# Optimization experiments

Measured on AMD Instinct MI355X. Metric: run time of the kernel, lower is better.

The kernel has to match this reference:

```python
import jax, jax.numpy as jnp
import numpy as np

N_NODES = 500_000
N_EDGES = 16_000_000


def setup_inputs() -> dict:
    key = jax.random.key(0)
    ks = jax.random.split(key, 16)
    x = jax.random.normal(ks[0], (N_NODES, 4), dtype=jnp.float32)
    edge_index = jax.random.randint(ks[1], (2, N_EDGES), 0, N_NODES, dtype=jnp.int64)

    def lin(k, out_dim, in_dim):
        # kaiming-uniform-ish init like torch Linear
        bound = 1.0 / np.sqrt(in_dim)
        return jax.random.uniform(k, (out_dim, in_dim), jnp.float32, -bound, bound)

    def bias(k, out_dim, in_dim):
        bound = 1.0 / np.sqrt(in_dim)
        return jax.random.uniform(k, (out_dim,), jnp.float32, -bound, bound)

    return {
        "x": x,
        "edge_index": edge_index,
        # SAGEConv1: 4 -> 10  (lin_l acts on aggregated neighbors, has bias; lin_r on self, no bias)
        "w1l": lin(ks[2], 10, 4), "b1": bias(ks[3], 10, 4), "w1r": lin(ks[4], 10, 4),
        # SAGEConv2: 10 -> 20
        "w2l": lin(ks[5], 20, 10), "b2": bias(ks[6], 20, 10), "w2r": lin(ks[7], 20, 10),
        # SAGEConv3: 20 -> 20
        "w3l": lin(ks[8], 20, 20), "b3": bias(ks[9], 20, 20), "w3r": lin(ks[10], 20, 20),
        # classifier: 20 -> 8
        "wc": lin(ks[11], 8, 20), "bc": bias(ks[12], 8, 20),
    }


def _sage_conv(h, src, dst, deg_inv, wl, bl, wr):
    # mean-aggregate neighbor features: messages flow src -> dst
    msg = h[src]                                   # [E, F] gather
    agg = jax.ops.segment_sum(msg, dst, num_segments=N_NODES)  # [N, F]
    agg = agg * deg_inv                            # mean over in-neighbors
    return agg @ wl.T + bl + h @ wr.T              # lin_l(aggr) + lin_r(self)


def reference(x, edge_index, w1l, b1, w1r, w2l, b2, w2r, w3l, b3, w3r, wc, bc):
    src, dst = edge_index[0], edge_index[1]
    deg = jax.ops.segment_sum(jnp.ones((src.shape[0],), x.dtype), dst,
                              num_segments=N_NODES)
    deg_inv = (1.0 / jnp.maximum(deg, 1.0))[:, None]  # [N, 1]

    h = jax.nn.relu(_sage_conv(x, src, dst, deg_inv, w1l, b1, w1r))
    h = jax.nn.relu(_sage_conv(h, src, dst, deg_inv, w2l, b2, w2r))
    h = jax.nn.relu(_sage_conv(h, src, dst, deg_inv, w3l, b3, w3r))
    return h @ wc.T + bc
```

## Files before the change

### kernel.cpp

```cpp
#include <hip/hip_runtime.h>
#include <hip/hip_fp16.h>

#define N_NODES 500000
#define N_EDGES 16000000
#define NB 1954
#define NPB_LOG 9
#define NPB 512
#define NBUCK 977
#define NBUCK_PAD 1024
#define CH 32768
#define NSB 489

#define SLICE_SHIFT 15
#define NSLICE 16
#define NKEY (NPB * NSLICE)

__device__ __forceinline__ float2 up2(int p) {
    __half2 h = *reinterpret_cast<__half2*>(&p);
    return __half22float2(h);
}
__device__ __forceinline__ int pk2(float a, float b) {
    __half2 h = __floats2half2_rn(a, b);
    return *reinterpret_cast<int*>(&h);
}


__global__ void bucket_hist(const int* __restrict__ dst, int* __restrict__ ghist) {
    __shared__ int lhist[NBUCK_PAD];
    for (int t = threadIdx.x; t < NBUCK_PAD; t += 256) lhist[t] = 0;
    __syncthreads();
    int stride = gridDim.x * 256;
    for (int i = blockIdx.x * 256 + threadIdx.x; i < N_EDGES; i += stride) {
        atomicAdd(&lhist[dst[i] >> NPB_LOG], 1);
    }
    __syncthreads();
    for (int t = threadIdx.x; t < NBUCK_PAD; t += 256) {
        int c = lhist[t];
        if (c) atomicAdd(&ghist[t], c);
    }
}

__global__ void bucket_scan(int* __restrict__ gcur, int* __restrict__ bbase) {
    __shared__ int s[256];
    int t = threadIdx.x;
    int v[4], sum = 0, loc[4];
#pragma unroll
    for (int j = 0; j < 4; ++j) {
        v[j] = gcur[t * 4 + j];
        loc[j] = sum;
        sum += v[j];
    }
    s[t] = sum;
    __syncthreads();
    for (int o = 1; o < 256; o <<= 1) {
        int x = (t >= o) ? s[t - o] : 0;
        __syncthreads();
// ... 77 lines not shown
    }
    __syncthreads();

#pragma unroll
    for (int j = 0; j < 2; ++j) {
        int idx = t + j * 256;
        int ng = node0 + idx;
        if (ng < N_NODES) off[ng] = bb + hist[idx << 4];
    }
    if (b == NBUCK - 1 && t == 0) off[N_NODES] = N_EDGES;
    __syncthreads();

    for (int j = bb + t; j < be; j += 256) {
        int p = P[j];
        int n = p >> 19;
        int s = p & 0x7FFFF;
        int pos = atomicAdd(&hist[(n << 4) | (s >> SLICE_SHIFT)], 1);
        S[bb + pos] = s;
    }
}


__global__ void convert_x(const float* __restrict__ x, int2* __restrict__ xh) {
    int i = blockIdx.x * 256 + threadIdx.x;
    if (i >= N_NODES) return;
    float4 v = ((const float4*)x)[i];
    int2 r;
    r.x = pk2(v.x, v.y);
    r.y = pk2(v.z, v.w);
    xh[i] = r;
}


__global__ __launch_bounds__(256, 4) void fused_l1(
        const int* __restrict__ off, const int* __restrict__ ssrc,
        const int2* __restrict__ xh, const float* __restrict__ x,
        const float* __restrict__ wl, const float* __restrict__ bl,
        const float* __restrict__ wr, int* __restrict__ h1) {
    __shared__ float s_wl[40];
    __shared__ float s_wr[40];
    __shared__ float s_b[10];
    if (threadIdx.x < 40) {
        s_wl[threadIdx.x] = wl[threadIdx.x];
        s_wr[threadIdx.x] = wr[threadIdx.x];
    }
    if (threadIdx.x >= 64 && threadIdx.x < 74) s_b[threadIdx.x - 64] = bl[threadIdx.x - 64];
    __syncthreads();

    int i = blockIdx.x * 256 + threadIdx.x;
    if (i >= N_NODES) return;

    int b = off[i], e = off[i + 1];
    constexpr int UN = 8;

    float acc[4] = {0.f, 0.f, 0.f, 0.f};

    int k = b;
    for (; k + UN - 1 < e; k += UN) {
        int sidx[UN];
#pragma unroll
        for (int u = 0; u < UN; ++u) sidx[u] = ssrc[k + u];
        int2 v[UN];
#pragma unroll
        for (int u = 0; u < UN; ++u) v[u] = xh[sidx[u]];
#pragma unroll
        for (int u = 0; u < UN; ++u) {
            float2 f0 = up2(v[u].x), f1 = up2(v[u].y);
            acc[0] += f0.x; acc[1] += f0.y; acc[2] += f1.x; acc[3] += f1.y;
        }
    }
    for (; k < e; ++k) {
        int2 v = xh[ssrc[k]];
        float2 f0 = up2(v.x), f1 = up2(v.y);
        acc[0] += f0.x; acc[1] += f0.y; acc[2] += f1.x; acc[3] += f1.y;
    }

    float inv = 1.f / fmaxf((float)(e - b), 1.f);
#pragma unroll
    for (int q = 0; q < 4; ++q) acc[q] *= inv;

    float4 xs = ((const float4*)x)[i];
    float xv[4] = {xs.x, xs.y, xs.z, xs.w};

    float r[10];
#pragma unroll
    for (int j = 0; j < 10; ++j) {
        float t = s_b[j];
#pragma unroll
        for (int kk = 0; kk < 4; ++kk) {
            t += s_wl[j * 4 + kk] * acc[kk] + s_wr[j * 4 + kk] * xv[kk];
        }
        r[j] = fmaxf(t, 0.f);
    }
    int4 o0;
    o0.x = pk2(r[0], r[1]); o0.y = pk2(r[2], r[3]);
    o0.z = pk2(r[4], r[5]); o0.w = pk2(r[6], r[7]);
    *(int4*)(h1 + (long)i * 8) = o0;
    h1[(long)i * 8 + 4] = pk2(r[8], r[9]);
}

__global__ __launch_bounds__(256, 4) void fused_l2(
        const int* __restrict__ off, const int* __restrict__ ssrc,
        const int* __restrict__ h1,
        const float* __restrict__ wl, const float* __restrict__ bl,
        const float* __restrict__ wr, int* __restrict__ h2) {
    __shared__ float s_wl[200];
    __shared__ float s_wr[200];
    __shared__ float s_b[20];
    if (threadIdx.x < 200) {
        s_wl[threadIdx.x] = wl[threadIdx.x];
        s_wr[threadIdx.x] = wr[threadIdx.x];
    }
    if (threadIdx.x >= 224 && threadIdx.x < 244) s_b[threadIdx.x - 224] = bl[threadIdx.x - 224];
    __syncthreads();

    int i = blockIdx.x * 256 + threadIdx.x;
    if (i >= N_NODES) return;

    int b = off[i], e = off[i + 1];
    constexpr int UN = 4;

    float acc[10];
#pragma unroll
    for (int q = 0; q < 10; ++q) acc[q] = 0.f;

    int k = b;
    for (; k + UN - 1 < e; k += UN) {
        int sidx[UN];
#pragma unroll
        for (int u = 0; u < UN; ++u) sidx[u] = ssrc[k + u];
        int4 v4[UN];
        int v1[UN];
#pragma unroll
        for (int u = 0; u < UN; ++u) {
            const int* row = h1 + (long)sidx[u] * 8;
            v4[u] = *(const int4*)row;
            v1[u] = row[4];
        }
#pragma unroll
        for (int u = 0; u < UN; ++u) {
            float2 f0 = up2(v4[u].x), f1 = up2(v4[u].y), f2 = up2(v4[u].z), f3 = up2(v4[u].w), f4 = up2(v1[u]);
            acc[0] += f0.x; acc[1] += f0.y; acc[2] += f1.x; acc[3] += f1.y;
            acc[4] += f2.x; acc[5] += f2.y; acc[6] += f3.x; acc[7] += f3.y;
            acc[8] += f4.x; acc[9] += f4.y;
        }
    }
    for (; k < e; ++k) {
        const int* row = h1 + (long)ssrc[k] * 8;
        int4 v4 = *(const int4*)row;
        int v1 = row[4];
        float2 f0 = up2(v4.x), f1 = up2(v4.y), f2 = up2(v4.z), f3 = up2(v4.w), f4 = up2(v1);
        acc[0] += f0.x; acc[1] += f0.y; acc[2] += f1.x; acc[3] += f1.y;
        acc[4] += f2.x; acc[5] += f2.y; acc[6] += f3.x; acc[7] += f3.y;
        acc[8] += f4.x; acc[9] += f4.y;
    }

    float inv = 1.f / fmaxf((float)(e - b), 1.f);
#pragma unroll
    for (int q = 0; q < 10; ++q) acc[q] *= inv;

    float xv[10];
    {
        const int* row = h1 + (long)i * 8;
        int4 v4 = *(const int4*)row;
        int v1 = row[4];
        float2 f0 = up2(v4.x), f1 = up2(v4.y), f2 = up2(v4.z), f3 = up2(v4.w), f4 = up2(v1);
        xv[0] = f0.x; xv[1] = f0.y; xv[2] = f1.x; xv[3] = f1.y;
        xv[4] = f2.x; xv[5] = f2.y; xv[6] = f3.x; xv[7] = f3.y;
        xv[8] = f4.x; xv[9] = f4.y;
    }

    float r[20];
#pragma unroll
    for (int j = 0; j < 20; ++j) {
        float t = s_b[j];
#pragma unroll
        for (int kk = 0; kk < 10; ++kk) {
            t += s_wl[j * 10 + kk] * acc[kk] + s_wr[j * 10 + kk] * xv[kk];
        }
        r[j] = fmaxf(t, 0.f);
    }
    int* o = h2 + (long)i * 16;
    int4 o0, o1;
    o0.x = pk2(r[0], r[1]);   o0.y = pk2(r[2], r[3]);
    o0.z = pk2(r[4], r[5]);   o0.w = pk2(r[6], r[7]);
    o1.x = pk2(r[8], r[9]);   o1.y = pk2(r[10], r[11]);
    o1.z = pk2(r[12], r[13]); o1.w = pk2(r[14], r[15]);
    *(int4*)o = o0;
    *(int4*)(o + 4) = o1;
    int2 o2;
    o2.x = pk2(r[16], r[17]); o2.y = pk2(r[18], r[19]);
    *(int2*)(o + 8) = o2;
}

__global__ __launch_bounds__(256, 4) void fused_l3(
        const int* __restrict__ off, const int* __restrict__ ssrc,
        const int* __restrict__ h2,
        const float* __restrict__ w3l, const float* __restrict__ b3,
        const float* __restrict__ w3r,
        const float* __restrict__ wc, const float* __restrict__ bc,
        float* __restrict__ out) {
    __shared__ float s_wl[400];
    __shared__ float s_wr[400];
    __shared__ float s_b[20];
    __shared__ float s_wc[160];
    __shared__ float s_bc[8];
    for (int t = threadIdx.x; t < 400; t += 256) {
        s_wl[t] = w3l[t];
        s_wr[t] = w3r[t];
    }
    if (threadIdx.x < 160) s_wc[threadIdx.x] = wc[threadIdx.x];
    if (threadIdx.x >= 192 && threadIdx.x < 212) s_b[threadIdx.x - 192] = b3[threadIdx.x - 192];
    if (threadIdx.x >= 224 && threadIdx.x < 232) s_bc[threadIdx.x - 224] = bc[threadIdx.x - 224];
    __syncthreads();

    int i = blockIdx.x * 256 + threadIdx.x;
    if (i >= N_NODES) return;

    int b = off[i], e = off[i + 1];
    constexpr int UN = 4;

    float acc[20];
#pragma unroll
    for (int q = 0; q < 20; ++q) acc[q] = 0.f;

    int k = b;
    for (; k + UN - 1 < e; k += UN) {
        int sidx[UN];
#pragma unroll
        for (int u = 0; u < UN; ++u) sidx[u] = ssrc[k + u];
        int4 va[UN], vb[UN];
        int2 vc[UN];
#pragma unroll
        for (int u = 0; u < UN; ++u) {
            const int* row = h2 + (long)sidx[u] * 16;
            va[u] = *(const int4*)row;
            vb[u] = *(const int4*)(row + 4);
            vc[u] = *(const int2*)(row + 8);
        }
#pragma unroll
        for (int u = 0; u < UN; ++u) {
            float2 f;
            f = up2(va[u].x); acc[0] += f.x; acc[1] += f.y;
            f = up2(va[u].y); acc[2] += f.x; acc[3] += f.y;
            f = up2(va[u].z); acc[4] += f.x; acc[5] += f.y;
            f = up2(va[u].w); acc[6] += f.x; acc[7] += f.y;
            f = up2(vb[u].x); acc[8] += f.x; acc[9] += f.y;
            f = up2(vb[u].y); acc[10] += f.x; acc[11] += f.y;
            f = up2(vb[u].z); acc[12] += f.x; acc[13] += f.y;
            f = up2(vb[u].w); acc[14] += f.x; acc[15] += f.y;
            f = up2(vc[u].x); acc[16] += f.x; acc[17] += f.y;
            f = up2(vc[u].y); acc[18] += f.x; acc[19] += f.y;
        }
    }
    for (; k < e; ++k) {
        const int* row = h2 + (long)ssrc[k] * 16;
        int4 va = *(const int4*)row;
        int4 vb = *(const int4*)(row + 4);
        int2 vc = *(const int2*)(row + 8);
        float2 f;
        f = up2(va.x); acc[0] += f.x; acc[1] += f.y;
        f = up2(va.y); acc[2] += f.x; acc[3] += f.y;
        f = up2(va.z); acc[4] += f.x; acc[5] += f.y;
        f = up2(va.w); acc[6] += f.x; acc[7] += f.y;
        f = up2(vb.x); acc[8] += f.x; acc[9] += f.y;
        f = up2(vb.y); acc[10] += f.x; acc[11] += f.y;
        f = up2(vb.z); acc[12] += f.x; acc[13] += f.y;
        f = up2(vb.w); acc[14] += f.x; acc[15] += f.y;
        f = up2(vc.x); acc[16] += f.x; acc[17] += f.y;
        f = up2(vc.y); acc[18] += f.x; acc[19] += f.y;
    }

    float inv = 1.f / fmaxf((float)(e - b), 1.f);
#pragma unroll
    for (int q = 0; q < 20; ++q) acc[q] *= inv;

    float xv[20];
    {
        const int* row = h2 + (long)i * 16;
        int4 va = *(const int4*)row;
        int4 vb = *(const int4*)(row + 4);
        int2 vc = *(const int2*)(row + 8);
        float2 f;
        f = up2(va.x); xv[0] = f.x; xv[1] = f.y;
        f = up2(va.y); xv[2] = f.x; xv[3] = f.y;
        f = up2(va.z); xv[4] = f.x; xv[5] = f.y;
        f = up2(va.w); xv[6] = f.x; xv[7] = f.y;
        f = up2(vb.x); xv[8] = f.x; xv[9] = f.y;
        f = up2(vb.y); xv[10] = f.x; xv[11] = f.y;
        f = up2(vb.z); xv[12] = f.x; xv[13] = f.y;
        f = up2(vb.w); xv[14] = f.x; xv[15] = f.y;
        f = up2(vc.x); xv[16] = f.x; xv[17] = f.y;
        f = up2(vc.y); xv[18] = f.x; xv[19] = f.y;
    }

    float h3[20];
#pragma unroll
    for (int j = 0; j < 20; ++j) {
        float r = s_b[j];
#pragma unroll
        for (int kk = 0; kk < 20; ++kk) {
            r += s_wl[j * 20 + kk] * acc[kk] + s_wr[j * 20 + kk] * xv[kk];
        }
        h3[j] = fmaxf(r, 0.f);
    }
#pragma unroll
    for (int j = 0; j < 8; ++j) {
        float r = s_bc[j];
#pragma unroll
        for (int kk = 0; kk < 20; ++kk) {
            r += s_wc[j * 20 + kk] * h3[kk];
        }
        out[(long)i * 8 + j] = r;
    }
}


__global__ void deg_kernel(const int* __restrict__ dst, int* __restrict__ deg) {
    int i = blockIdx.x * blockDim.x + threadIdx.x;
    if (i < N_EDGES) atomicAdd(&deg[dst[i]], 1);
}

template <int F>
__global__ void edge_agg(const int* __restrict__ src, const int* __restrict__ dst,
                         const float* __restrict__ h, float* __restrict__ agg) {
    int i = blockIdx.x * blockDim.x + threadIdx.x;
    if (i >= N_EDGES) return;
    int s = src[i];
    int d = dst[i];
    const float* hs = h + (long)s * F;
    float* ad = agg + (long)d * F;
#pragma unroll
    for (int f = 0; f < F; ++f) atomicAdd(&ad[f], hs[f]);
}

template <int FIN, int FOUT>
__global__ void node_apply(const float* __restrict__ agg, const float* __restrict__ hin,
                           const int* __restrict__ deg, const float* __restrict__ wl,
                           const float* __restrict__ bl, const float* __restrict__ wr,
                           float* __restrict__ hout) {
    __shared__ float s_wl[FOUT * FIN];
    __shared__ float s_wr[FOUT * FIN];
    __shared__ float s_b[FOUT];
    for (int t = threadIdx.x; t < FOUT * FIN; t += blockDim.x) {
        s_wl[t] = wl[t];
        s_wr[t] = wr[t];
    }
// ... 69 lines not shown
    const int* ei = (const int*)d_in[1];
    const float* w1l = (const float*)d_in[2];
    const float* b1 = (const float*)d_in[3];
    const float* w1r = (const float*)d_in[4];
    const float* w2l = (const float*)d_in[5];
    const float* b2 = (const float*)d_in[6];
    const float* w2r = (const float*)d_in[7];
    const float* w3l = (const float*)d_in[8];
    const float* b3 = (const float*)d_in[9];
    const float* w3r = (const float*)d_in[10];
    const float* wc = (const float*)d_in[11];
    const float* bc = (const float*)d_in[12];
    float* out = (float*)d_out;

    const int* src = ei;
    const int* dst = ei + N_EDGES;

    const int BT = 256;
    dim3 blk(BT);
    dim3 egrid((N_EDGES + BT - 1) / BT);
    dim3 ngrid(NB);

    const size_t NEED_A = 130008448;

    if (ws_size >= NEED_A) {
        char* ws = (char*)d_ws;
        int* off = (int*)ws;
        int* bbase = (int*)(ws + 2000128);
        int* gcur = (int*)(ws + 2004352);
        int* P = (int*)(ws + 2008448);
        int2* xh = (int2*)(ws + 2008448);
        int* h1 = (int*)(ws + 6008448);
        int* h2 = (int*)(ws + 22008448);
        int* S = (int*)(ws + 66008448);

        hipMemsetAsync(gcur, 0, NBUCK_PAD * sizeof(int), stream);
        bucket_hist<<<1024, blk, 0, stream>>>(dst, gcur);
        bucket_scan<<<1, blk, 0, stream>>>(gcur, bbase);
        bucket_scatter<<<NSB, blk, 0, stream>>>(src, dst, gcur, P);
        fine_sort<<<NBUCK, blk, 0, stream>>>(P, bbase, off, S);

        convert_x<<<ngrid, blk, 0, stream>>>(x, xh);
        fused_l1<<<ngrid, blk, 0, stream>>>(off, S, xh, x, w1l, b1, w1r, h1);
        fused_l2<<<ngrid, blk, 0, stream>>>(off, S, h1, w2l, b2, w2r, h2);
        fused_l3<<<ngrid, blk, 0, stream>>>(off, S, h2, w3l, b3, w3r, wc, bc, out);
    } else {
        char* ws = (char*)d_ws;
        int* deg = (int*)ws;
        float* agg = (float*)(ws + 2000000);
        float* h1 = (float*)(ws + 42000000);
        float* h2 = (float*)(ws + 62000000);

        hipMemsetAsync(deg, 0, (size_t)N_NODES * sizeof(int), stream);
        deg_kernel<<<egrid, blk, 0, stream>>>(dst, deg);

        hipMemsetAsync(agg, 0, (size_t)N_NODES * 4 * sizeof(float), stream);
        edge_agg<4><<<egrid, blk, 0, stream>>>(src, dst, x, agg);
        node_apply<4, 10><<<ngrid, blk, 0, stream>>>(agg, x, deg, w1l, b1, w1r, h1);

        hipMemsetAsync(agg, 0, (size_t)N_NODES * 10 * sizeof(float), stream);
        edge_agg<10><<<egrid, blk, 0, stream>>>(src, dst, h1, agg);
        node_apply<10, 20><<<ngrid, blk, 0, stream>>>(agg, h1, deg, w2l, b2, w2r, h2);

        hipMemsetAsync(agg, 0, (size_t)N_NODES * 20 * sizeof(float), stream);
        edge_agg<20><<<egrid, blk, 0, stream>>>(src, dst, h2, agg);
        node_final_old<<<ngrid, blk, 0, stream>>>(agg, h2, deg, w3l, b3, w3r, wc, bc, out);
    }
}
```

Measured before the change: 1.650 ms.

## Sweep source-node slices in lockstep across grid with soft barriers for cache locality

Replaces the three per-node gather kernels with persistent-style kernels of 1024 blocks, each thread handling two destination nodes. Threads walk their sorted neighbor lists one source slice at a time, and a relaxed soft grid barrier between slices keeps all blocks on the same slice of the feature table so the gathers stay cache-resident. The barrier gives up after a spin budget, so correctness does not depend on co-residency. The cost is spin-wait overhead and lower per-thread memory parallelism, since the unrolled batched loads become serial dependent loads.

```diff
diff --git a/kernel.cpp b/kernel.cpp
--- a/kernel.cpp
+++ b/kernel.cpp
@@ -15,6 +15,9 @@
 #define NSLICE 16
 #define NKEY (NPB * NSLICE)
 
+#define GRID_BLK 1024
+#define NTHREADS (GRID_BLK * 256)
+
 __device__ __forceinline__ float2 up2(int p) {
     __half2 h = *reinterpret_cast<__half2*>(&p);
     return __half22float2(h);
@@ -22,6 +25,17 @@
 __device__ __forceinline__ int pk2(float a, float b) {
     __half2 h = __floats2half2_rn(a, b);
     return *reinterpret_cast<int*>(&h);
+}
+
+__device__ __forceinline__ bool grid_phase_barrier(int* bar, int idx, int budget, bool wait) {
+    __hip_atomic_fetch_add(&bar[idx], 1, __ATOMIC_RELAXED, __HIP_MEMORY_SCOPE_AGENT);
+    if (!wait) return false;
+    int spins = 0;
+    while (__hip_atomic_load(&bar[idx], __ATOMIC_RELAXED, __HIP_MEMORY_SCOPE_AGENT) < GRID_BLK) {
+        if (++spins > budget) return false;
+        __builtin_amdgcn_s_sleep(16);
+    }
+    return true;
 }
 
 
@@ -165,11 +179,38 @@
 }
 
 
-__global__ __launch_bounds__(256, 4) void fused_l1(
+__device__ __forceinline__ void l1_tail(int n, float deg, const float* acc,
+        const float* __restrict__ x, const float* s_wl, const float* s_wr,
+        const float* s_b, int* __restrict__ h1) {
+    if (n >= N_NODES) return;
+    float inv = 1.f / fmaxf(deg, 1.f);
+    float a[4];
+#pragma unroll
+    for (int q = 0; q < 4; ++q) a[q] = acc[q] * inv;
+    float4 xs = ((const float4*)x)[n];
+    float xv[4] = {xs.x, xs.y, xs.z, xs.w};
+    float r[10];
+#pragma unroll
+    for (int j = 0; j < 10; ++j) {
+        float t = s_b[j];
+#pragma unroll
+        for (int kk = 0; kk < 4; ++kk)
+            t += s_wl[j * 4 + kk] * a[kk] + s_wr[j * 4 + kk] * xv[kk];
+        r[j] = fmaxf(t, 0.f);
+    }
+    int4 o0;
+    o0.x = pk2(r[0], r[1]); o0.y = pk2(r[2], r[3]);
+    o0.z = pk2(r[4], r[5]); o0.w = pk2(r[6], r[7]);
+    *(int4*)(h1 + (long)n * 8) = o0;
+    h1[(long)n * 8 + 4] = pk2(r[8], r[9]);
+}
+
+__global__ __launch_bounds__(256, 4) void fused_l1p(
         const int* __restrict__ off, const int* __restrict__ ssrc,
         const int2* __restrict__ xh, const float* __restrict__ x,
         const float* __restrict__ wl, const float* __restrict__ bl,
-        const float* __restrict__ wr, int* __restrict__ h1) {
+        const float* __restrict__ wr, int* __restrict__ h1,
+        int* __restrict__ bar) {
     __shared__ float s_wl[40];
     __shared__ float s_wr[40];
     __shared__ float s_b[10];
@@ -180,121 +221,55 @@
     if (threadIdx.x >= 64 && threadIdx.x < 74) s_b[threadIdx.x - 64] = bl[threadIdx.x - 64];
     __syncthreads();
 
-    int i = blockIdx.x * 256 + threadIdx.x;
-    if (i >= N_NODES) return;
-
-    int b = off[i], e = off[i + 1];
-    constexpr int UN = 8;
-
-    float acc[4] = {0.f, 0.f, 0.f, 0.f};
-
-    int k = b;
-    for (; k + UN - 1 < e; k += UN) {
-        int sidx[UN];
-#pragma unroll
-        for (int u = 0; u < UN; ++u) sidx[u] = ssrc[k + u];
-        int2 v[UN];
-#pragma unroll
-        for (int u = 0; u < UN; ++u) v[u] = xh[sidx[u]];
-#pragma unroll
-        for (int u = 0; u < UN; ++u) {
-            float2 f0 = up2(v[u].x), f1 = up2(v[u].y);
-            acc[0] += f0.x; acc[1] += f0.y; acc[2] += f1.x; acc[3] += f1.y;
-        }
-    }
-    for (; k < e; ++k) {
-        int2 v = xh[ssrc[k]];
-        float2 f0 = up2(v.x), f1 = up2(v.y);
-        acc[0] += f0.x; acc[1] += f0.y; acc[2] += f1.x; acc[3] += f1.y;
-    }
-
-    float inv = 1.f / fmaxf((float)(e - b), 1.f);
-#pragma unroll
-    for (int q = 0; q < 4; ++q) acc[q] *= inv;
-
-    float4 xs = ((const float4*)x)[i];
-    float xv[4] = {xs.x, xs.y, xs.z, xs.w};
-
-    float r[10];
-#pragma unroll
-    for (int j = 0; j < 10; ++j) {
-        float t = s_b[j];
-#pragma unroll
-        for (int kk = 0; kk < 4; ++kk) {
-            t += s_wl[j * 4 + kk] * acc[kk] + s_wr[j * 4 + kk] * xv[kk];
-        }
-        r[j] = fmaxf(t, 0.f);
-    }
-    int4 o0;
-    o0.x = pk2(r[0], r[1]); o0.y = pk2(r[2], r[3]);
-    o0.z = pk2(r[4], r[5]); o0.w = pk2(r[6], r[7]);
-    *(int4*)(h1 + (long)i * 8) = o0;
-    h1[(long)i * 8 + 4] = pk2(r[8], r[9]);
-}
-
-__global__ __launch_bounds__(256, 4) void fused_l2(
-        const int* __restrict__ off, const int* __restrict__ ssrc,
-        const int* __restrict__ h1,
-        const float* __restrict__ wl, const float* __restrict__ bl,
-        const float* __restrict__ wr, int* __restrict__ h2) {
-    __shared__ float s_wl[200];
-    __shared__ float s_wr[200];
-    __shared__ float s_b[20];
-    if (threadIdx.x < 200) {
-        s_wl[threadIdx.x] = wl[threadIdx.x];
-        s_wr[threadIdx.x] = wr[threadIdx.x];
-    }
-    if (threadIdx.x >= 224 && threadIdx.x < 244) s_b[threadIdx.x - 224] = bl[threadIdx.x - 224];
-    __syncthreads();
-
-    int i = blockIdx.x * 256 + threadIdx.x;
-    if (i >= N_NODES) return;
-
-    int b = off[i], e = off[i + 1];
-    constexpr int UN = 4;
-
-    float acc[10];
-#pragma unroll
-    for (int q = 0; q < 10; ++q) acc[q] = 0.f;
-
-    int k = b;
-    for (; k + UN - 1 < e; k += UN) {
-        int sidx[UN];
-#pragma unroll
-        for (int u = 0; u < UN; ++u) sidx[u] = ssrc[k + u];
-        int4 v4[UN];
-        int v1[UN];
-#pragma unroll
-        for (int u = 0; u < UN; ++u) {
-            const int* row = h1 + (long)sidx[u] * 8;
-            v4[u] = *(const int4*)row;
-            v1[u] = row[4];
-        }
-#pragma unroll
-        for (int u = 0; u < UN; ++u) {
-            float2 f0 = up2(v4[u].x), f1 = up2(v4[u].y), f2 = up2(v4[u].z), f3 = up2(v4[u].w), f4 = up2(v1[u]);
-            acc[0] += f0.x; acc[1] += f0.y; acc[2] += f1.x; acc[3] += f1.y;
-            acc[4] += f2.x; acc[5] += f2.y; acc[6] += f3.x; acc[7] += f3.y;
-            acc[8] += f4.x; acc[9] += f4.y;
-        }
-    }
-    for (; k < e; ++k) {
-        const int* row = h1 + (long)ssrc[k] * 8;
-        int4 v4 = *(const int4*)row;
-        int v1 = row[4];
-        float2 f0 = up2(v4.x), f1 = up2(v4.y), f2 = up2(v4.z), f3 = up2(v4.w), f4 = up2(v1);
-        acc[0] += f0.x; acc[1] += f0.y; acc[2] += f1.x; acc[3] += f1.y;
-        acc[4] += f2.x; acc[5] += f2.y; acc[6] += f3.x; acc[7] += f3.y;
-        acc[8] += f4.x; acc[9] += f4.y;
-    }
-
-    float inv = 1.f / fmaxf((float)(e - b), 1.f);
+    const int tg = blockIdx.x * 256 + threadIdx.x;
+    const int n0 = tg, n1 = tg + NTHREADS;
+    int k0 = off[n0], e0 = off[n0 + 1];
+    int k1 = 0, e1 = 0;
+    if (n1 < N_NODES) { k1 = off[n1]; e1 = off[n1 + 1]; }
+    float deg0 = (float)(e0 - k0), deg1 = (float)(e1 - k1);
+    int sv0 = (k0 < e0) ? ssrc[k0] : 0x7FFFFFFF;
+    int sv1 = (k1 < e1) ? ssrc[k1] : 0x7FFFFFFF;
+    float acc0[4] = {0.f, 0.f, 0.f, 0.f};
+    float acc1[4] = {0.f, 0.f, 0.f, 0.f};
+
+    bool coop = true;
+    if (threadIdx.x == 0) coop = grid_phase_barrier(bar, 16, 300, true);
+    __syncthreads();
+
+    constexpr int PH = 8, SPP = NSLICE / PH;
+    for (int s = 0; s < PH; ++s) {
+        const int lim = ((s + 1) * SPP) << SLICE_SHIFT;
+        while (sv0 < lim) {
+            int2 v = xh[sv0];
+            ++k0; sv0 = (k0 < e0) ? ssrc[k0] : 0x7FFFFFFF;
+            float2 f0 = up2(v.x), f1 = up2(v.y);
+            acc0[0] += f0.x; acc0[1] += f0.y; acc0[2] += f1.x; acc0[3] += f1.y;
+        }
+        while (sv1 < lim) {
+            int2 v = xh[sv1];
+            ++k1; sv1 = (k1 < e1) ? ssrc[k1] : 0x7FFFFFFF;
+            float2 f0 = up2(v.x), f1 = up2(v.y);
+            acc1[0] += f0.x; acc1[1] += f0.y; acc1[2] += f1.x; acc1[3] += f1.y;
+        }
+        if (s < PH - 1) {
+            if (threadIdx.x == 0) coop = grid_phase_barrier(bar, s, 60, coop) && coop;
+            __syncthreads();
+        }
+    }
+    l1_tail(n0, deg0, acc0, x, s_wl, s_wr, s_b, h1);
+    l1_tail(n1, deg1, acc1, x, s_wl, s_wr, s_b, h1);
+}
+
+__device__ __forceinline__ void l2_tail(int n, float deg, float* acc,
+        const int* __restrict__ h1, const float* s_wl, const float* s_wr,
+        const float* s_b, int* __restrict__ h2) {
+    if (n >= N_NODES) return;
+    float inv = 1.f / fmaxf(deg, 1.f);
 #pragma unroll
     for (int q = 0; q < 10; ++q) acc[q] *= inv;
-
     float xv[10];
     {
-        const int* row = h1 + (long)i * 8;
+        const int* row = h1 + (long)n * 8;
         int4 v4 = *(const int4*)row;
         int v1 = row[4];
         float2 f0 = up2(v4.x), f1 = up2(v4.y), f2 = up2(v4.z), f3 = up2(v4.w), f4 = up2(v1);
@@ -302,18 +277,16 @@
         xv[4] = f2.x; xv[5] = f2.y; xv[6] = f3.x; xv[7] = f3.y;
         xv[8] = f4.x; xv[9] = f4.y;
     }
-
     float r[20];
 #pragma unroll
     for (int j = 0; j < 20; ++j) {
         float t = s_b[j];
 #pragma unroll
-        for (int kk = 0; kk < 10; ++kk) {
+        for (int kk = 0; kk < 10; ++kk)
             t += s_wl[j * 10 + kk] * acc[kk] + s_wr[j * 10 + kk] * xv[kk];
-        }
         r[j] = fmaxf(t, 0.f);
     }
-    int* o = h2 + (long)i * 16;
+    int* o = h2 + (long)n * 16;
     int4 o0, o1;
     o0.x = pk2(r[0], r[1]);   o0.y = pk2(r[2], r[3]);
     o0.z = pk2(r[4], r[5]);   o0.w = pk2(r[6], r[7]);
@@ -326,91 +299,81 @@
     *(int2*)(o + 8) = o2;
 }
 
-__global__ __launch_bounds__(256, 4) void fused_l3(
+__global__ __launch_bounds__(256, 4) void fused_l2p(
         const int* __restrict__ off, const int* __restrict__ ssrc,
-        const int* __restrict__ h2,
-        const float* __restrict__ w3l, const float* __restrict__ b3,
-        const float* __restrict__ w3r,
-        const float* __restrict__ wc, const float* __restrict__ bc,
+        const int* __restrict__ h1,
+        const float* __restrict__ wl, const float* __restrict__ bl,
+        const float* __restrict__ wr, int* __restrict__ h2,
+        int* __restrict__ bar) {
+    __shared__ float s_wl[200];
+    __shared__ float s_wr[200];
+    __shared__ float s_b[20];
+    if (threadIdx.x < 200) {
+        s_wl[threadIdx.x] = wl[threadIdx.x];
+        s_wr[threadIdx.x] = wr[threadIdx.x];
+    }
+    if (threadIdx.x >= 224 && threadIdx.x < 244) s_b[threadIdx.x - 224] = bl[threadIdx.x - 224];
+    __syncthreads();
+
+    const int tg = blockIdx.x * 256 + threadIdx.x;
+    const int n0 = tg, n1 = tg + NTHREADS;
+    int k0 = off[n0], e0 = off[n0 + 1];
+    int k1 = 0, e1 = 0;
+    if (n1 < N_NODES) { k1 = off[n1]; e1 = off[n1 + 1]; }
+    float deg0 = (float)(e0 - k0), deg1 = (float)(e1 - k1);
+    int sv0 = (k0 < e0) ? ssrc[k0] : 0x7FFFFFFF;
+    int sv1 = (k1 < e1) ? ssrc[k1] : 0x7FFFFFFF;
+    float acc0[10], acc1[10];
+#pragma unroll
+    for (int q = 0; q < 10; ++q) { acc0[q] = 0.f; acc1[q] = 0.f; }
+
+    bool coop = true;
+    if (threadIdx.x == 0) coop = grid_phase_barrier(bar, 16, 300, true);
+    __syncthreads();
+
+    constexpr int PH = 8, SPP = NSLICE / PH;
+    for (int s = 0; s < PH; ++s) {
+        const int lim = ((s + 1) * SPP) << SLICE_SHIFT;
+        while (sv0 < lim) {
+            const int* row = h1 + (long)sv0 * 8;
+            int4 v4 = *(const int4*)row;
+            int v1 = row[4];
+            ++k0; sv0 = (k0 < e0) ? ssrc[k0] : 0x7FFFFFFF;
+            float2 f0 = up2(v4.x), f1 = up2(v4.y), f2 = up2(v4.z), f3 = up2(v4.w), f4 = up2(v1);
+            acc0[0] += f0.x; acc0[1] += f0.y; acc0[2] += f1.x; acc0[3] += f1.y;
+            acc0[4] += f2.x; acc0[5] += f2.y; acc0[6] += f3.x; acc0[7] += f3.y;
+            acc0[8] += f4.x; acc0[9] += f4.y;
+        }
+        while (sv1 < lim) {
+            const int* row = h1 + (long)sv1 * 8;
+            int4 v4 = *(const int4*)row;
+            int v1 = row[4];
+            ++k1; sv1 = (k1 < e1) ? ssrc[k1] : 0x7FFFFFFF;
+            float2 f0 = up2(v4.x), f1 = up2(v4.y), f2 = up2(v4.z), f3 = up2(v4.w), f4 = up2(v1);
+            acc1[0] += f0.x; acc1[1] += f0.y; acc1[2] += f1.x; acc1[3] += f1.y;
+            acc1[4] += f2.x; acc1[5] += f2.y; acc1[6] += f3.x; acc1[7] += f3.y;
+            acc1[8] += f4.x; acc1[9] += f4.y;
+        }
+        if (s < PH - 1) {
+            if (threadIdx.x == 0) coop = grid_phase_barrier(bar, s, 60, coop) && coop;
+            __syncthreads();
+        }
+    }
+    l2_tail(n0, deg0, acc0, h1, s_wl, s_wr, s_b, h2);
+    l2_tail(n1, deg1, acc1, h1, s_wl, s_wr, s_b, h2);
+}
+
+__device__ __forceinline__ void l3_tail(int n, float deg, float* acc,
+        const int* __restrict__ h2, const float* s_wl, const float* s_wr,
+        const float* s_b, const float* s_wc, const float* s_bc,
         float* __restrict__ out) {
-    __shared__ float s_wl[400];
-    __shared__ float s_wr[400];
-    __shared__ float s_b[20];
-    __shared__ float s_wc[160];
-    __shared__ float s_bc[8];
-    for (int t = threadIdx.x; t < 400; t += 256) {
-        s_wl[t] = w3l[t];
-        s_wr[t] = w3r[t];
-    }
-    if (threadIdx.x < 160) s_wc[threadIdx.x] = wc[threadIdx.x];
-    if (threadIdx.x >= 192 && threadIdx.x < 212) s_b[threadIdx.x - 192] = b3[threadIdx.x - 192];
-    if (threadIdx.x >= 224 && threadIdx.x < 232) s_bc[threadIdx.x - 224] = bc[threadIdx.x - 224];
-    __syncthreads();
-
-    int i = blockIdx.x * 256 + threadIdx.x;
-    if (i >= N_NODES) return;
-
-    int b = off[i], e = off[i + 1];
-    constexpr int UN = 4;
-
-    float acc[20];
-#pragma unroll
-    for (int q = 0; q < 20; ++q) acc[q] = 0.f;
-
-    int k = b;
-    for (; k + UN - 1 < e; k += UN) {
-        int sidx[UN];
-#pragma unroll
-        for (int u = 0; u < UN; ++u) sidx[u] = ssrc[k + u];
-        int4 va[UN], vb[UN];
-        int2 vc[UN];
-#pragma unroll
-        for (int u = 0; u < UN; ++u) {
-            const int* row = h2 + (long)sidx[u] * 16;
-            va[u] = *(const int4*)row;
-            vb[u] = *(const int4*)(row + 4);
-            vc[u] = *(const int2*)(row + 8);
-        }
-#pragma unroll
-        for (int u = 0; u < UN; ++u) {
-            float2 f;
-            f = up2(va[u].x); acc[0] += f.x; acc[1] += f.y;
-            f = up2(va[u].y); acc[2] += f.x; acc[3] += f.y;
-            f = up2(va[u].z); acc[4] += f.x; acc[5] += f.y;
-            f = up2(va[u].w); acc[6] += f.x; acc[7] += f.y;
-            f = up2(vb[u].x); acc[8] += f.x; acc[9] += f.y;
-            f = up2(vb[u].y); acc[10] += f.x; acc[11] += f.y;
-            f = up2(vb[u].z); acc[12] += f.x; acc[13] += f.y;
-            f = up2(vb[u].w); acc[14] += f.x; acc[15] += f.y;
-            f = up2(vc[u].x); acc[16] += f.x; acc[17] += f.y;
-            f = up2(vc[u].y); acc[18] += f.x; acc[19] += f.y;
-        }
-    }
-    for (; k < e; ++k) {
-        const int* row = h2 + (long)ssrc[k] * 16;
-        int4 va = *(const int4*)row;
-        int4 vb = *(const int4*)(row + 4);
-        int2 vc = *(const int2*)(row + 8);
-        float2 f;
-        f = up2(va.x); acc[0] += f.x; acc[1] += f.y;
-        f = up2(va.y); acc[2] += f.x; acc[3] += f.y;
-        f = up2(va.z); acc[4] += f.x; acc[5] += f.y;
-        f = up2(va.w); acc[6] += f.x; acc[7] += f.y;
-        f = up2(vb.x); acc[8] += f.x; acc[9] += f.y;
-        f = up2(vb.y); acc[10] += f.x; acc[11] += f.y;
-        f = up2(vb.z); acc[12] += f.x; acc[13] += f.y;
-        f = up2(vb.w); acc[14] += f.x; acc[15] += f.y;
-        f = up2(vc.x); acc[16] += f.x; acc[17] += f.y;
-        f = up2(vc.y); acc[18] += f.x; acc[19] += f.y;
-    }
-
-    float inv = 1.f / fmaxf((float)(e - b), 1.f);
+    if (n >= N_NODES) return;
+    float inv = 1.f / fmaxf(deg, 1.f);
 #pragma unroll
     for (int q = 0; q < 20; ++q) acc[q] *= inv;
-
     float xv[20];
     {
-        const int* row = h2 + (long)i * 16;
+        const int* row = h2 + (long)n * 16;
         int4 va = *(const int4*)row;
         int4 vb = *(const int4*)(row + 4);
         int2 vc = *(const int2*)(row + 8);
@@ -426,26 +389,107 @@
         f = up2(vc.x); xv[16] = f.x; xv[17] = f.y;
         f = up2(vc.y); xv[18] = f.x; xv[19] = f.y;
     }
-
     float h3[20];
 #pragma unroll
     for (int j = 0; j < 20; ++j) {
         float r = s_b[j];
 #pragma unroll
-        for (int kk = 0; kk < 20; ++kk) {
+        for (int kk = 0; kk < 20; ++kk)
             r += s_wl[j * 20 + kk] * acc[kk] + s_wr[j * 20 + kk] * xv[kk];
-        }
         h3[j] = fmaxf(r, 0.f);
     }
 #pragma unroll
     for (int j = 0; j < 8; ++j) {
         float r = s_bc[j];
 #pragma unroll
-        for (int kk = 0; kk < 20; ++kk) {
-            r += s_wc[j * 20 + kk] * h3[kk];
-        }
-        out[(long)i * 8 + j] = r;
-    }
+        for (int kk = 0; kk < 20; ++kk) r += s_wc[j * 20 + kk] * h3[kk];
+        out[(long)n * 8 + j] = r;
+    }
+}
+
+__global__ __launch_bounds__(256, 4) void fused_l3p(
+        const int* __restrict__ off, const int* __restrict__ ssrc,
+        const int* __restrict__ h2,
+        const float* __restrict__ w3l, const float* __restrict__ b3,
+        const float* __restrict__ w3r,
+        const float* __restrict__ wc, const float* __restrict__ bc,
+        float* __restrict__ out, int* __restrict__ bar) {
+    __shared__ float s_wl[400];
+    __shared__ float s_wr[400];
+    __shared__ float s_b[20];
+    __shared__ float s_wc[160];
+    __shared__ float s_bc[8];
+    for (int t = threadIdx.x; t < 400; t += 256) {
+        s_wl[t] = w3l[t];
+        s_wr[t] = w3r[t];
+    }
+    if (threadIdx.x < 160) s_wc[threadIdx.x] = wc[threadIdx.x];
+    if (threadIdx.x >= 192 && threadIdx.x < 212) s_b[threadIdx.x - 192] = b3[threadIdx.x - 192];
+    if (threadIdx.x >= 224 && threadIdx.x < 232) s_bc[threadIdx.x - 224] = bc[threadIdx.x - 224];
+    __syncthreads();
+
+    const int tg = blockIdx.x * 256 + threadIdx.x;
+    const int n0 = tg, n1 = tg + NTHREADS;
+    int k0 = off[n0], e0 = off[n0 + 1];
+    int k1 = 0, e1 = 0;
+    if (n1 < N_NODES) { k1 = off[n1]; e1 = off[n1 + 1]; }
+    float deg0 = (float)(e0 - k0), deg1 = (float)(e1 - k1);
+    int sv0 = (k0 < e0) ? ssrc[k0] : 0x7FFFFFFF;
+    int sv1 = (k1 < e1) ? ssrc[k1] : 0x7FFFFFFF;
+    float acc0[20], acc1[20];
+#pragma unroll
+    for (int q = 0; q < 20; ++q) { acc0[q] = 0.f; acc1[q] = 0.f; }
+
+    bool coop = true;
+    if (threadIdx.x == 0) coop = grid_phase_barrier(bar, 16, 300, true);
+    __syncthreads();
+
+    constexpr int PH = 16;
+    for (int s = 0; s < PH; ++s) {
+        const int lim = (s + 1) << SLICE_SHIFT;
+        while (sv0 < lim) {
+            const int* row = h2 + (long)sv0 * 16;
+            int4 va = *(const int4*)row;
+            int4 vb = *(const int4*)(row + 4);
+            int2 vc = *(const int2*)(row + 8);
+            ++k0; sv0 = (k0 < e0) ? ssrc[k0] : 0x7FFFFFFF;
+            float2 f;
+            f = up2(va.x); acc0[0] += f.x; acc0[1] += f.y;
+            f = up2(va.y); acc0[2] += f.x; acc0[3] += f.y;
+            f = up2(va.z); acc0[4] += f.x; acc0[5] += f.y;
+            f = up2(va.w); acc0[6] += f.x; acc0[7] += f.y;
+            f = up2(vb.x); acc0[8] += f.x; acc0[9] += f.y;
+            f = up2(vb.y); acc0[10] += f.x; acc0[11] += f.y;
+            f = up2(vb.z); acc0[12] += f.x; acc0[13] += f.y;
+            f = up2(vb.w); acc0[14] += f.x; acc0[15] += f.y;
+            f = up2(vc.x); acc0[16] += f.x; acc0[17] += f.y;
+            f = up2(vc.y); acc0[18] += f.x; acc0[19] += f.y;
+        }
+        while (sv1 < lim) {
+            const int* row = h2 + (long)sv1 * 16;
+            int4 va = *(const int4*)row;
+            int4 vb = *(const int4*)(row + 4);
+            int2 vc = *(const int2*)(row + 8);
+            ++k1; sv1 = (k1 < e1) ? ssrc[k1] : 0x7FFFFFFF;
+            float2 f;
+            f = up2(va.x); acc1[0] += f.x; acc1[1] += f.y;
+            f = up2(va.y); acc1[2] += f.x; acc1[3] += f.y;
+            f = up2(va.z); acc1[4] += f.x; acc1[5] += f.y;
+            f = up2(va.w); acc1[6] += f.x; acc1[7] += f.y;
+            f = up2(vb.x); acc1[8] += f.x; acc1[9] += f.y;
+            f = up2(vb.y); acc1[10] += f.x; acc1[11] += f.y;
+            f = up2(vb.z); acc1[12] += f.x; acc1[13] += f.y;
+            f = up2(vb.w); acc1[14] += f.x; acc1[15] += f.y;
+            f = up2(vc.x); acc1[16] += f.x; acc1[17] += f.y;
+            f = up2(vc.y); acc1[18] += f.x; acc1[19] += f.y;
+        }
+        if (s < PH - 1) {
+            if (threadIdx.x == 0) coop = grid_phase_barrier(bar, s, 60, coop) && coop;
+            __syncthreads();
+        }
+    }
+    l3_tail(n0, deg0, acc0, h2, s_wl, s_wr, s_b, s_wc, s_bc, out);
+    l3_tail(n1, deg1, acc1, h2, s_wl, s_wr, s_b, s_wc, s_bc, out);
 }
 
 
@@ -589,10 +633,12 @@
         bucket_scatter<<<NSB, blk, 0, stream>>>(src, dst, gcur, P);
         fine_sort<<<NBUCK, blk, 0, stream>>>(P, bbase, off, S);
 
+        hipMemsetAsync(gcur, 0, 128 * sizeof(int), stream);
+
         convert_x<<<ngrid, blk, 0, stream>>>(x, xh);
-        fused_l1<<<ngrid, blk, 0, stream>>>(off, S, xh, x, w1l, b1, w1r, h1);
-        fused_l2<<<ngrid, blk, 0, stream>>>(off, S, h1, w2l, b2, w2r, h2);
-        fused_l3<<<ngrid, blk, 0, stream>>>(off, S, h2, w3l, b3, w3r, wc, bc, out);
+        fused_l1p<<<GRID_BLK, blk, 0, stream>>>(off, S, xh, x, w1l, b1, w1r, h1, gcur);
+        fused_l2p<<<GRID_BLK, blk, 0, stream>>>(off, S, h1, w2l, b2, w2r, h2, gcur + 32);
+        fused_l3p<<<GRID_BLK, blk, 0, stream>>>(off, S, h2, w3l, b3, w3r, wc, bc, out, gcur + 64);
     } else {
         char* ws = (char*)d_ws;
         int* deg = (int*)ws;
```

Result: slower. 3.862 ms (+134.0%).

## Phase neighbor gathers by source slice with soft grid barriers for cache locality

Applied to the files above, without the earlier changes.

Layers 2 and 3 now run as a persistent 1024-block grid where each thread handles two nodes. The sorted neighbor lists are walked in phases bounded by source-index slices, with a timeout-based grid barrier between phases. This keeps all blocks gathering from the same slice of the feature table at once so those rows stay in cache, instead of random gathers across the whole table. In exchange it adds barrier spin overhead and halves the node parallelism per thread. If blocks are not co-resident, the barrier budgets time out and the kernels fall back to unsynchronized gathers.

```diff
diff --git a/kernel.cpp b/kernel.cpp
--- a/kernel.cpp
+++ b/kernel.cpp
@@ -15,6 +15,17 @@
 #define NSLICE 16
 #define NKEY (NPB * NSLICE)
 
+#define GRID_BLK 1024
+#define HALF_T (GRID_BLK * 256)
+
+#define BAR_SUBC 16
+#define BAR_SUBQ (GRID_BLK / BAR_SUBC)
+#define BAR_REC_INTS 1024
+#define BAR_MASTER 512
+#define BAR_FLAG 544
+#define ENTRY_BUDGET 1500
+#define PHASE_BUDGET 400
+
 __device__ __forceinline__ float2 up2(int p) {
     __half2 h = *reinterpret_cast<__half2*>(&p);
     return __half22float2(h);
@@ -22,6 +33,27 @@
 __device__ __forceinline__ int pk2(float a, float b) {
     __half2 h = __floats2half2_rn(a, b);
     return *reinterpret_cast<int*>(&h);
+}
+
+__device__ __forceinline__ void barrier_arrive(int* rec, int bid) {
+    int r = __hip_atomic_fetch_add(&rec[(bid & (BAR_SUBC - 1)) * 32], 1,
+                                   __ATOMIC_RELAXED, __HIP_MEMORY_SCOPE_AGENT);
+    if (r == BAR_SUBQ - 1) {
+        int mr = __hip_atomic_fetch_add(&rec[BAR_MASTER], 1,
+                                        __ATOMIC_RELAXED, __HIP_MEMORY_SCOPE_AGENT);
+        if (mr == BAR_SUBC - 1)
+            __hip_atomic_store(&rec[BAR_FLAG], 1,
+                               __ATOMIC_RELAXED, __HIP_MEMORY_SCOPE_AGENT);
+    }
+}
+__device__ __forceinline__ bool barrier_wait(int* rec, int budget) {
+    int spins = 0;
+    while (__hip_atomic_load(&rec[BAR_FLAG],
+                             __ATOMIC_RELAXED, __HIP_MEMORY_SCOPE_AGENT) == 0) {
+        if (++spins > budget) return false;
+        __builtin_amdgcn_s_sleep(8);
+    }
+    return true;
 }
 
 
@@ -232,69 +264,92 @@
     h1[(long)i * 8 + 4] = pk2(r[8], r[9]);
 }
 
-__global__ __launch_bounds__(256, 4) void fused_l2(
-        const int* __restrict__ off, const int* __restrict__ ssrc,
-        const int* __restrict__ h1,
-        const float* __restrict__ wl, const float* __restrict__ bl,
-        const float* __restrict__ wr, int* __restrict__ h2) {
-    __shared__ float s_wl[200];
-    __shared__ float s_wr[200];
-    __shared__ float s_b[20];
-    if (threadIdx.x < 200) {
-        s_wl[threadIdx.x] = wl[threadIdx.x];
-        s_wr[threadIdx.x] = wr[threadIdx.x];
-    }
-    if (threadIdx.x >= 224 && threadIdx.x < 244) s_b[threadIdx.x - 224] = bl[threadIdx.x - 224];
-    __syncthreads();
-
-    int i = blockIdx.x * 256 + threadIdx.x;
-    if (i >= N_NODES) return;
-
-    int b = off[i], e = off[i + 1];
-    constexpr int UN = 4;
-
-    float acc[10];
-#pragma unroll
-    for (int q = 0; q < 10; ++q) acc[q] = 0.f;
-
-    int k = b;
-    for (; k + UN - 1 < e; k += UN) {
-        int sidx[UN];
-#pragma unroll
-        for (int u = 0; u < UN; ++u) sidx[u] = ssrc[k + u];
-        int4 v4[UN];
-        int v1[UN];
-#pragma unroll
-        for (int u = 0; u < UN; ++u) {
-            const int* row = h1 + (long)sidx[u] * 8;
-            v4[u] = *(const int4*)row;
-            v1[u] = row[4];
+
+__device__ __forceinline__ void l2_scan_phase(int& k, const int e, const int lim,
+        const int* __restrict__ ssrc, const int* __restrict__ h1, float* acc) {
+    while (k < e) {
+        int sidx[4];
+#pragma unroll
+        for (int u = 0; u < 4; ++u)
+            sidx[u] = (k + u < e) ? ssrc[k + u] : 0x7FFFFFFF;
+        int m = (sidx[0] < lim) + (sidx[1] < lim) + (sidx[2] < lim) + (sidx[3] < lim);
+        if (m == 0) return;
+        int4 v4[4];
+        int v1[4];
+#pragma unroll
+        for (int u = 0; u < 4; ++u) {
+            if (u < m) {
+                const int* row = h1 + (long)sidx[u] * 8;
+                v4[u] = *(const int4*)row;
+                v1[u] = row[4];
+            }
         }
 #pragma unroll
-        for (int u = 0; u < UN; ++u) {
-            float2 f0 = up2(v4[u].x), f1 = up2(v4[u].y), f2 = up2(v4[u].z), f3 = up2(v4[u].w), f4 = up2(v1[u]);
-            acc[0] += f0.x; acc[1] += f0.y; acc[2] += f1.x; acc[3] += f1.y;
-            acc[4] += f2.x; acc[5] += f2.y; acc[6] += f3.x; acc[7] += f3.y;
-            acc[8] += f4.x; acc[9] += f4.y;
+        for (int u = 0; u < 4; ++u) {
+            if (u < m) {
+                float2 f0 = up2(v4[u].x), f1 = up2(v4[u].y), f2 = up2(v4[u].z),
+                       f3 = up2(v4[u].w), f4 = up2(v1[u]);
+                acc[0] += f0.x; acc[1] += f0.y; acc[2] += f1.x; acc[3] += f1.y;
+                acc[4] += f2.x; acc[5] += f2.y; acc[6] += f3.x; acc[7] += f3.y;
+                acc[8] += f4.x; acc[9] += f4.y;
+            }
         }
-    }
-    for (; k < e; ++k) {
-        const int* row = h1 + (long)ssrc[k] * 8;
-        int4 v4 = *(const int4*)row;
-        int v1 = row[4];
-        float2 f0 = up2(v4.x), f1 = up2(v4.y), f2 = up2(v4.z), f3 = up2(v4.w), f4 = up2(v1);
-        acc[0] += f0.x; acc[1] += f0.y; acc[2] += f1.x; acc[3] += f1.y;
-        acc[4] += f2.x; acc[5] += f2.y; acc[6] += f3.x; acc[7] += f3.y;
-        acc[8] += f4.x; acc[9] += f4.y;
-    }
-
-    float inv = 1.f / fmaxf((float)(e - b), 1.f);
+        k += m;
+        if (m < 4) return;
+    }
+}
+
+__device__ __forceinline__ void l3_scan_phase(int& k, const int e, const int lim,
+        const int* __restrict__ ssrc, const int* __restrict__ h2, float* acc) {
+    while (k < e) {
+        int sidx[4];
+#pragma unroll
+        for (int u = 0; u < 4; ++u)
+            sidx[u] = (k + u < e) ? ssrc[k + u] : 0x7FFFFFFF;
+        int m = (sidx[0] < lim) + (sidx[1] < lim) + (sidx[2] < lim) + (sidx[3] < lim);
+        if (m == 0) return;
+        int4 va[4], vb[4];
+        int2 vc[4];
+#pragma unroll
+        for (int u = 0; u < 4; ++u) {
+            if (u < m) {
+                const int* row = h2 + (long)sidx[u] * 16;
+                va[u] = *(const int4*)row;
+                vb[u] = *(const int4*)(row + 4);
+                vc[u] = *(const int2*)(row + 8);
+            }
+        }
+#pragma unroll
+        for (int u = 0; u < 4; ++u) {
+            if (u < m) {
+                float2 f;
+                f = up2(va[u].x); acc[0] += f.x; acc[1] += f.y;
+                f = up2(va[u].y); acc[2] += f.x; acc[3] += f.y;
+                f = up2(va[u].z); acc[4] += f.x; acc[5] += f.y;
+                f = up2(va[u].w); acc[6] += f.x; acc[7] += f.y;
+                f = up2(vb[u].x); acc[8] += f.x; acc[9] += f.y;
+                f = up2(vb[u].y); acc[10] += f.x; acc[11] += f.y;
+                f = up2(vb[u].z); acc[12] += f.x; acc[13] += f.y;
+                f = up2(vb[u].w); acc[14] += f.x; acc[15] += f.y;
+                f = up2(vc[u].x); acc[16] += f.x; acc[17] += f.y;
+                f = up2(vc[u].y); acc[18] += f.x; acc[19] += f.y;
+            }
+        }
+        k += m;
+        if (m < 4) return;
+    }
+}
+
+__device__ __forceinline__ void l2_tail(int n, float deg, float* acc,
+        const int* __restrict__ h1, const float* s_wl, const float* s_wr,
+        const float* s_b, int* __restrict__ h2) {
+    if (n >= N_NODES) return;
+    float inv = 1.f / fmaxf(deg, 1.f);
 #pragma unroll
     for (int q = 0; q < 10; ++q) acc[q] *= inv;
-
     float xv[10];
     {
-        const int* row = h1 + (long)i * 8;
+        const int* row = h1 + (long)n * 8;
         int4 v4 = *(const int4*)row;
         int v1 = row[4];
         float2 f0 = up2(v4.x), f1 = up2(v4.y), f2 = up2(v4.z), f3 = up2(v4.w), f4 = up2(v1);
@@ -302,18 +357,16 @@
         xv[4] = f2.x; xv[5] = f2.y; xv[6] = f3.x; xv[7] = f3.y;
         xv[8] = f4.x; xv[9] = f4.y;
     }
-
     float r[20];
 #pragma unroll
     for (int j = 0; j < 20; ++j) {
         float t = s_b[j];
 #pragma unroll
-        for (int kk = 0; kk < 10; ++kk) {
+        for (int kk = 0; kk < 10; ++kk)
             t += s_wl[j * 10 + kk] * acc[kk] + s_wr[j * 10 + kk] * xv[kk];
-        }
         r[j] = fmaxf(t, 0.f);
     }
-    int* o = h2 + (long)i * 16;
+    int* o = h2 + (long)n * 16;
     int4 o0, o1;
     o0.x = pk2(r[0], r[1]);   o0.y = pk2(r[2], r[3]);
     o0.z = pk2(r[4], r[5]);   o0.w = pk2(r[6], r[7]);
@@ -326,91 +379,68 @@
     *(int2*)(o + 8) = o2;
 }
 
-__global__ __launch_bounds__(256, 4) void fused_l3(
+__global__ __launch_bounds__(256, 4) void fused_l2p(
         const int* __restrict__ off, const int* __restrict__ ssrc,
-        const int* __restrict__ h2,
-        const float* __restrict__ w3l, const float* __restrict__ b3,
-        const float* __restrict__ w3r,
-        const float* __restrict__ wc, const float* __restrict__ bc,
+        const int* __restrict__ h1,
+        const float* __restrict__ wl, const float* __restrict__ bl,
+        const float* __restrict__ wr, int* __restrict__ h2,
+        int* __restrict__ bar) {
+    __shared__ float s_wl[200];
+    __shared__ float s_wr[200];
+    __shared__ float s_b[20];
+    if (threadIdx.x < 200) {
+        s_wl[threadIdx.x] = wl[threadIdx.x];
+        s_wr[threadIdx.x] = wr[threadIdx.x];
+    }
+    if (threadIdx.x >= 224 && threadIdx.x < 244) s_b[threadIdx.x - 224] = bl[threadIdx.x - 224];
+    __syncthreads();
+
+    const int tg = blockIdx.x * 256 + threadIdx.x;
+    const int n0 = tg, n1 = tg + HALF_T;
+    int k0 = off[n0], e0 = off[n0 + 1];
+    int k1 = 0, e1 = 0;
+    if (n1 < N_NODES) { k1 = off[n1]; e1 = off[n1 + 1]; }
+    float deg0 = (float)(e0 - k0), deg1 = (float)(e1 - k1);
+    float acc0[10], acc1[10];
+#pragma unroll
+    for (int q = 0; q < 10; ++q) { acc0[q] = 0.f; acc1[q] = 0.f; }
+
+    bool coop = true;
+    if (threadIdx.x == 0) {
+        barrier_arrive(bar, blockIdx.x);
+        coop = barrier_wait(bar, ENTRY_BUDGET);
+    }
+    __syncthreads();
+
+    constexpr int PH = 8;
+    for (int s = 0; s < PH; ++s) {
+        const int lim = (s + 1) << (SLICE_SHIFT + 1);
+        l2_scan_phase(k0, e0, lim, ssrc, h1, acc0);
+        l2_scan_phase(k1, e1, lim, ssrc, h1, acc1);
+        if (s < PH - 1) {
+            if (threadIdx.x == 0) {
+                int* rec = bar + (1 + s) * BAR_REC_INTS;
+                barrier_arrive(rec, blockIdx.x);
+                if (coop) coop = barrier_wait(rec, PHASE_BUDGET);
+            }
+            __syncthreads();
+        }
+    }
+    l2_tail(n0, deg0, acc0, h1, s_wl, s_wr, s_b, h2);
+    l2_tail(n1, deg1, acc1, h1, s_wl, s_wr, s_b, h2);
+}
+
+__device__ __forceinline__ void l3_tail(int n, float deg, float* acc,
+        const int* __restrict__ h2, const float* s_wl, const float* s_wr,
+        const float* s_b, const float* s_wc, const float* s_bc,
         float* __restrict__ out) {
-    __shared__ float s_wl[400];
-    __shared__ float s_wr[400];
-    __shared__ float s_b[20];
-    __shared__ float s_wc[160];
-    __shared__ float s_bc[8];
-    for (int t = threadIdx.x; t < 400; t += 256) {
-        s_wl[t] = w3l[t];
-        s_wr[t] = w3r[t];
-    }
-    if (threadIdx.x < 160) s_wc[threadIdx.x] = wc[threadIdx.x];
-    if (threadIdx.x >= 192 && threadIdx.x < 212) s_b[threadIdx.x - 192] = b3[threadIdx.x - 192];
-    if (threadIdx.x >= 224 && threadIdx.x < 232) s_bc[threadIdx.x - 224] = bc[threadIdx.x - 224];
-    __syncthreads();
-
-    int i = blockIdx.x * 256 + threadIdx.x;
-    if (i >= N_NODES) return;
-
-    int b = off[i], e = off[i + 1];
-    constexpr int UN = 4;
-
-    float acc[20];
-#pragma unroll
-    for (int q = 0; q < 20; ++q) acc[q] = 0.f;
-
-    int k = b;
-    for (; k + UN - 1 < e; k += UN) {
-        int sidx[UN];
-#pragma unroll
-        for (int u = 0; u < UN; ++u) sidx[u] = ssrc[k + u];
-        int4 va[UN], vb[UN];
-        int2 vc[UN];
-#pragma unroll
-        for (int u = 0; u < UN; ++u) {
-            const int* row = h2 + (long)sidx[u] * 16;
-            va[u] = *(const int4*)row;
-            vb[u] = *(const int4*)(row + 4);
-            vc[u] = *(const int2*)(row + 8);
-        }
-#pragma unroll
-        for (int u = 0; u < UN; ++u) {
-            float2 f;
-            f = up2(va[u].x); acc[0] += f.x; acc[1] += f.y;
-            f = up2(va[u].y); acc[2] += f.x; acc[3] += f.y;
-            f = up2(va[u].z); acc[4] += f.x; acc[5] += f.y;
-            f = up2(va[u].w); acc[6] += f.x; acc[7] += f.y;
-            f = up2(vb[u].x); acc[8] += f.x; acc[9] += f.y;
-            f = up2(vb[u].y); acc[10] += f.x; acc[11] += f.y;
-            f = up2(vb[u].z); acc[12] += f.x; acc[13] += f.y;
-            f = up2(vb[u].w); acc[14] += f.x; acc[15] += f.y;
-            f = up2(vc[u].x); acc[16] += f.x; acc[17] += f.y;
-            f = up2(vc[u].y); acc[18] += f.x; acc[19] += f.y;
-        }
-    }
-    for (; k < e; ++k) {
-        const int* row = h2 + (long)ssrc[k] * 16;
-        int4 va = *(const int4*)row;
-        int4 vb = *(const int4*)(row + 4);
-        int2 vc = *(const int2*)(row + 8);
-        float2 f;
-        f = up2(va.x); acc[0] += f.x; acc[1] += f.y;
-        f = up2(va.y); acc[2] += f.x; acc[3] += f.y;
-        f = up2(va.z); acc[4] += f.x; acc[5] += f.y;
-        f = up2(va.w); acc[6] += f.x; acc[7] += f.y;
-        f = up2(vb.x); acc[8] += f.x; acc[9] += f.y;
-        f = up2(vb.y); acc[10] += f.x; acc[11] += f.y;
-        f = up2(vb.z); acc[12] += f.x; acc[13] += f.y;
-        f = up2(vb.w); acc[14] += f.x; acc[15] += f.y;
-        f = up2(vc.x); acc[16] += f.x; acc[17] += f.y;
-        f = up2(vc.y); acc[18] += f.x; acc[19] += f.y;
-    }
-
-    float inv = 1.f / fmaxf((float)(e - b), 1.f);
+    if (n >= N_NODES) return;
+    float inv = 1.f / fmaxf(deg, 1.f);
 #pragma unroll
     for (int q = 0; q < 20; ++q) acc[q] *= inv;
-
     float xv[20];
     {
-        const int* row = h2 + (long)i * 16;
+        const int* row = h2 + (long)n * 16;
         int4 va = *(const int4*)row;
         int4 vb = *(const int4*)(row + 4);
         int2 vc = *(const int2*)(row + 8);
@@ -426,26 +456,78 @@
         f = up2(vc.x); xv[16] = f.x; xv[17] = f.y;
         f = up2(vc.y); xv[18] = f.x; xv[19] = f.y;
     }
-
     float h3[20];
 #pragma unroll
     for (int j = 0; j < 20; ++j) {
         float r = s_b[j];
 #pragma unroll
-        for (int kk = 0; kk < 20; ++kk) {
+        for (int kk = 0; kk < 20; ++kk)
             r += s_wl[j * 20 + kk] * acc[kk] + s_wr[j * 20 + kk] * xv[kk];
-        }
         h3[j] = fmaxf(r, 0.f);
     }
 #pragma unroll
     for (int j = 0; j < 8; ++j) {
         float r = s_bc[j];
 #pragma unroll
-        for (int kk = 0; kk < 20; ++kk) {
-            r += s_wc[j * 20 + kk] * h3[kk];
+        for (int kk = 0; kk < 20; ++kk) r += s_wc[j * 20 + kk] * h3[kk];
+        out[(long)n * 8 + j] = r;
+    }
+}
+
+__global__ __launch_bounds__(256, 4) void fused_l3p(
+        const int* __restrict__ off, const int* __restrict__ ssrc,
+        const int* __restrict__ h2,
+        const float* __restrict__ w3l, const float* __restrict__ b3,
+        const float* __restrict__ w3r,
+        const float* __restrict__ wc, const float* __restrict__ bc,
+        float* __restrict__ out, int* __restrict__ bar) {
+    __shared__ float s_wl[400];
+    __shared__ float s_wr[400];
+    __shared__ float s_b[20];
+    __shared__ float s_wc[160];
+    __shared__ float s_bc[8];
+    for (int t = threadIdx.x; t < 400; t += 256) {
+        s_wl[t] = w3l[t];
+        s_wr[t] = w3r[t];
+    }
+    if (threadIdx.x < 160) s_wc[threadIdx.x] = wc[threadIdx.x];
+    if (threadIdx.x >= 192 && threadIdx.x < 212) s_b[threadIdx.x - 192] = b3[threadIdx.x - 192];
+    if (threadIdx.x >= 224 && threadIdx.x < 232) s_bc[threadIdx.x - 224] = bc[threadIdx.x - 224];
+    __syncthreads();
+
+    const int tg = blockIdx.x * 256 + threadIdx.x;
+    const int n0 = tg, n1 = tg + HALF_T;
+    int k0 = off[n0], e0 = off[n0 + 1];
+    int k1 = 0, e1 = 0;
+    if (n1 < N_NODES) { k1 = off[n1]; e1 = off[n1 + 1]; }
+    float deg0 = (float)(e0 - k0), deg1 = (float)(e1 - k1);
+    float acc0[20], acc1[20];
+#pragma unroll
+    for (int q = 0; q < 20; ++q) { acc0[q] = 0.f; acc1[q] = 0.f; }
+
+    bool coop = true;
+    if (threadIdx.x == 0) {
+        barrier_arrive(bar, blockIdx.x);
+        coop = barrier_wait(bar, ENTRY_BUDGET);
+    }
+    __syncthreads();
+
+    constexpr int PH = 16;
+    for (int s = 0; s < PH; ++s) {
+        const int lim = (s + 1) << SLICE_SHIFT;
+        l3_scan_phase(k0, e0, lim, ssrc, h2, acc0);
+        l3_scan_phase(k1, e1, lim, ssrc, h2, acc1);
+        if (s < PH - 1) {
+            if (threadIdx.x == 0) {
+                int* rec = bar + (1 + s) * BAR_REC_INTS;
+                barrier_arrive(rec, blockIdx.x);
+                if (coop) coop = barrier_wait(rec, PHASE_BUDGET);
+            }
+            __syncthreads();
         }
-        out[(long)i * 8 + j] = r;
-    }
+    }
+    l3_tail(n0, deg0, acc0, h2, s_wl, s_wr, s_b, s_wc, s_bc, out);
+    l3_tail(n1, deg1, acc1, h2, s_wl, s_wr, s_b, s_wc, s_bc, out);
 }
 
 
@@ -581,6 +663,8 @@
         int2* xh = (int2*)(ws + 2008448);
         int* h1 = (int*)(ws + 6008448);
         int* h2 = (int*)(ws + 22008448);
+        int* bar2 = (int*)(ws + 54008448);
+        int* bar3 = bar2 + 8 * BAR_REC_INTS;
         int* S = (int*)(ws + 66008448);
 
         hipMemsetAsync(gcur, 0, NBUCK_PAD * sizeof(int), stream);
@@ -589,10 +673,12 @@
         bucket_scatter<<<NSB, blk, 0, stream>>>(src, dst, gcur, P);
         fine_sort<<<NBUCK, blk, 0, stream>>>(P, bbase, off, S);
 
+        hipMemsetAsync(bar2, 0, 24 * BAR_REC_INTS * sizeof(int), stream);
+
         convert_x<<<ngrid, blk, 0, stream>>>(x, xh);
         fused_l1<<<ngrid, blk, 0, stream>>>(off, S, xh, x, w1l, b1, w1r, h1);
-        fused_l2<<<ngrid, blk, 0, stream>>>(off, S, h1, w2l, b2, w2r, h2);
-        fused_l3<<<ngrid, blk, 0, stream>>>(off, S, h2, w3l, b3, w3r, wc, bc, out);
+        fused_l2p<<<GRID_BLK, blk, 0, stream>>>(off, S, h1, w2l, b2, w2r, h2, bar2);
+        fused_l3p<<<GRID_BLK, blk, 0, stream>>>(off, S, h2, w3l, b3, w3r, wc, bc, out, bar3);
     } else {
         char* ws = (char*)d_ws;
         int* deg = (int*)ws;
```

After: 1.652 ms. About the same (+0.1%).
